# Optimization experiments

Hardware: AMD Instinct MI355X
Metric: run time of the kernel (lower is better)

The kernel has to match this reference:

```python
import jax, jax.numpy as jnp
import numpy as np

DIM = 2048
NUM_EXPERTS = 64
TOP_K = 2


def setup_inputs() -> dict:
    key = jax.random.key(0)
    kx, kw = jax.random.split(key)
    x = jax.random.normal(kx, (4, 8192, DIM), dtype=jnp.float32)
    # nn.Linear(dim, num_experts, bias=False) -> weight [num_experts, dim]
    W = jax.random.normal(kw, (NUM_EXPERTS, DIM), dtype=jnp.float32) * (1.0 / np.sqrt(DIM))
    return {"x": x, "W": W}


def reference(x, W):
    # gate scores: [B, S, E]
    gate_scores = jnp.einsum("bsd,ed->bse", x, W)
    # top-k over experts
    top_k_values, top_k_indices = jax.lax.top_k(gate_scores, TOP_K)
    top_k_weights = jax.nn.softmax(top_k_values, axis=-1)  # [B, S, K]
    # load-balancing aux loss
    expert_usage = jax.nn.softmax(gate_scores, axis=-1).mean(axis=(0, 1))  # [E]
    aux_loss = NUM_EXPERTS * jnp.sum(expert_usage ** 2)
    return (top_k_indices, top_k_weights, aux_loss)
```

## Files before the change

### kernel.cpp

```cpp
#include <hip/hip_runtime.h>

#define DIM   2048
#define NE    64
#define NTOK  32768
#define BM    64
#define NTHR  256
#define KW    (DIM/4)
#define BK    32
#define NKT   (KW/BK)
#define S     68

struct SmemGemm { float xs[4][BK*S]; float ws[4][BK*S]; };
struct SmemEpi  { float ps[4][BM*S]; float mx[BM]; float zinv[BM]; float us[4][NE]; };
union  Smem     { SmemGemm g; SmemEpi e; };

__global__ __launch_bounds__(NTHR, 2)
void router_main(const float* __restrict__ x, const float* __restrict__ W,
                 float* __restrict__ out_idx, float* __restrict__ out_w,
                 float* __restrict__ gusage)
{
    __shared__ Smem sm;
    const int tid  = threadIdx.x;
    const int w    = tid >> 6;
    const int ln   = tid & 63;
    const int tok0 = blockIdx.x * BM;
    const int a    = ln & 7;
    const int b    = ln >> 3;

    const float* xr = x + (size_t)(tok0 + ln) * DIM + w * KW;
    const float* wr = W + (size_t)ln * DIM + w * KW;

    float* xs = sm.g.xs[w];
    float* ws = sm.g.ws[w];

    float4 px[8], pw[8];
#pragma unroll
    for (int j = 0; j < 8; ++j) {
        px[j] = *(const float4*)(xr + 4*j);
        pw[j] = *(const float4*)(wr + 4*j);
    }

    float acc[8][8];
#pragma unroll
    for (int i = 0; i < 8; ++i)
#pragma unroll
        for (int jj = 0; jj < 8; ++jj) acc[i][jj] = 0.f;

    for (int kt = 0; kt < NKT; ++kt) {
#pragma unroll
        for (int j = 0; j < 8; ++j) {
            const int k = 4*j;
            xs[(k+0)*S + ln] = px[j].x;
            xs[(k+1)*S + ln] = px[j].y;
            xs[(k+2)*S + ln] = px[j].z;
            xs[(k+3)*S + ln] = px[j].w;
            ws[(k+0)*S + ln] = pw[j].x;
            ws[(k+1)*S + ln] = pw[j].y;
            ws[(k+2)*S + ln] = pw[j].z;
            ws[(k+3)*S + ln] = pw[j].w;
        }
        if (kt + 1 < NKT) {
            const int off = (kt + 1) * BK;
#pragma unroll
            for (int j = 0; j < 8; ++j) {
                px[j] = *(const float4*)(xr + off + 4*j);
                pw[j] = *(const float4*)(wr + off + 4*j);
            }
        }
#pragma unroll 4
        for (int dk = 0; dk < BK; ++dk) {
            const float4 a0 = *(const float4*)&xs[dk*S + 8*a];
            const float4 a1 = *(const float4*)&xs[dk*S + 8*a + 4];
            const float4 b0 = *(const float4*)&ws[dk*S + 8*b];
            const float4 b1 = *(const float4*)&ws[dk*S + 8*b + 4];
            const float av[8] = {a0.x,a0.y,a0.z,a0.w,a1.x,a1.y,a1.z,a1.w};
            const float bv[8] = {b0.x,b0.y,b0.z,b0.w,b1.x,b1.y,b1.z,b1.w};
#pragma unroll
            for (int i = 0; i < 8; ++i)
#pragma unroll
                for (int jj = 0; jj < 8; ++jj)
                    acc[i][jj] += av[i] * bv[jj];
        }
    }

    __syncthreads();
    {
        float* ps = sm.e.ps[w];
#pragma unroll
        for (int i = 0; i < 8; ++i) {
            *(float4*)&ps[(8*a+i)*S + 8*b    ] = make_float4(acc[i][0],acc[i][1],acc[i][2],acc[i][3]);
            *(float4*)&ps[(8*a+i)*S + 8*b + 4] = make_float4(acc[i][4],acc[i][5],acc[i][6],acc[i][7]);
        }
    }
    __syncthreads();
    {
        const int t = tid & 63;
        const int q = tid >> 6;
        float* p0 = sm.e.ps[0];
#pragma unroll
        for (int e0 = 0; e0 < 16; ++e0) {
            const int idx = t*S + (q*16 + e0);
            p0[idx] += sm.e.ps[1][idx] + sm.e.ps[2][idx] + sm.e.ps[3][idx];
        }
    }
    __syncthreads();

    const float* sc = sm.e.ps[0];
    if (tid < BM) {
        const int t = tid;
        float v1 = -3.4e38f, v2 = -3.4e38f;
        int   i1 = 0, i2 = 0;
        for (int e = 0; e < NE; ++e) {
            float s = sc[t*S + e];
            if (s > v1)      { v2 = v1; i2 = i1; v1 = s; i1 = e; }
            else if (s > v2) { v2 = s;  i2 = e; }
        }
        float z = 0.f;
        for (int e = 0; e < NE; ++e) z += __expf(sc[t*S + e] - v1);
        sm.e.mx[t]   = v1;
        sm.e.zinv[t] = 1.f / z;

        const int gt = tok0 + t;
        out_idx[gt*2 + 0] = (float)i1;
        out_idx[gt*2 + 1] = (float)i2;
        float e21 = __expf(v2 - v1);
        float w1  = 1.f / (1.f + e21);
        out_w[gt*2 + 0] = w1;
        out_w[gt*2 + 1] = e21 * w1;
    }
    __syncthreads();

    {
        const int e = tid & 63;
        const int c = tid >> 6;
        float u = 0.f;
        const int tbeg = c * 16;
        for (int t = tbeg; t < tbeg + 16; ++t)
            u += __expf(sc[t*S + e] - sm.e.mx[t]) * sm.e.zinv[t];
        sm.e.us[c][e] = u;
    }
    __syncthreads();
    if (tid < NE) {
        float u = sm.e.us[0][tid] + sm.e.us[1][tid] + sm.e.us[2][tid] + sm.e.us[3][tid];
        atomicAdd(&gusage[tid], u);
    }
}

__global__ void router_finalize(const float* __restrict__ gusage, float* __restrict__ out_aux)
{
    const int e = threadIdx.x;
    float u = gusage[e] * (1.0f / (float)NTOK);
    float s = u * u;
#pragma unroll
    for (int off = 32; off > 0; off >>= 1)
        s += __shfl_down(s, off, 64);
    if (e == 0) out_aux[0] = (float)NE * s;
}

extern "C" void kernel_launch(void* const* d_in, const int* in_sizes, int n_in,
                              void* d_out, int out_size, void* d_ws, size_t ws_size,
                              hipStream_t stream)
{
    const float* x = (const float*)d_in[0];
    const float* W = (const float*)d_in[1];
    float* out     = (float*)d_out;
    float* out_idx = out;
    float* out_w   = out + NTOK * 2;
    float* out_aux = out + NTOK * 4;
    float* gusage  = (float*)d_ws;

    hipMemsetAsync(d_ws, 0, NE * sizeof(float), stream);
    hipLaunchKernelGGL(router_main, dim3(NTOK / BM), dim3(NTHR), 0, stream,
                       x, W, out_idx, out_w, gusage);
    hipLaunchKernelGGL(router_finalize, dim3(1), dim3(NE), 0, stream, gusage, out_aux);
}
```

Baseline: 407.0 us.

## Use split-bf16 MFMA (bf16x3/6-term) for router GEMM instead of FP32 FMA

Replaces the scalar FP32 shared-memory GEMM with MFMA bf16 instructions. Both x and W are split into three bf16 parts (high, mid, low) and six cross products are accumulated, so results stay close to FP32 accuracy. W is pre-split once per call by a new kernel into workspace planes, while x is split on the fly in registers and loaded straight from global memory without shared-memory staging. This trades extra MFMA work, conversion ALU and an extra launch for matrix-core throughput, with a small risk to exact top-k tie ordering.

```diff
diff --git a/kernel.cpp b/kernel.cpp
--- a/kernel.cpp
+++ b/kernel.cpp
@@ -1,111 +1,169 @@
 #include <hip/hip_runtime.h>
 
-#define DIM   2048
-#define NE    64
-#define NTOK  32768
-#define BM    64
-#define NTHR  256
-#define KW    (DIM/4)
-#define BK    32
-#define NKT   (KW/BK)
-#define S     68
-
-struct SmemGemm { float xs[4][BK*S]; float ws[4][BK*S]; };
-struct SmemEpi  { float ps[4][BM*S]; float mx[BM]; float zinv[BM]; float us[4][NE]; };
-union  Smem     { SmemGemm g; SmemEpi e; };
+#define DIM    2048
+#define NE     64
+#define NTOK   32768
+#define BM     64
+#define NTHR   256
+#define KW     512
+#define NKC    16
+#define S      68
+#define WPLANE (NE*DIM)
+
+typedef __attribute__((ext_vector_type(8))) short short8;
+typedef __attribute__((ext_vector_type(4))) float f32x4;
+
+union U4S8 { uint4 u; short8 s; };
+
+__device__ __forceinline__ unsigned pack_hi16(unsigned e0, unsigned e1) {
+    return __builtin_amdgcn_perm(e1, e0, 0x07060302u);
+}
+
+__device__ __forceinline__ void split8(const float4& a, const float4& b,
+                                       short8& h, short8& m, short8& l) {
+    const float f[8] = {a.x, a.y, a.z, a.w, b.x, b.y, b.z, b.w};
+    unsigned hb[8], mb[8], lb[8];
+#pragma unroll
+    for (int j = 0; j < 8; ++j) {
+        const unsigned xb = __float_as_uint(f[j]);
+        const unsigned th = xb & 0xffff0000u;
+        const float    rh = f[j] - __uint_as_float(th);
+        const unsigned rb = __float_as_uint(rh);
+        const unsigned tm = rb & 0xffff0000u;
+        const float    rm = rh - __uint_as_float(tm);
+        hb[j] = th; mb[j] = tm; lb[j] = __float_as_uint(rm);
+    }
+    U4S8 H, M, L;
+    H.u = make_uint4(pack_hi16(hb[0],hb[1]), pack_hi16(hb[2],hb[3]),
+                     pack_hi16(hb[4],hb[5]), pack_hi16(hb[6],hb[7]));
+    M.u = make_uint4(pack_hi16(mb[0],mb[1]), pack_hi16(mb[2],mb[3]),
+                     pack_hi16(mb[4],mb[5]), pack_hi16(mb[6],mb[7]));
+    L.u = make_uint4(pack_hi16(lb[0],lb[1]), pack_hi16(lb[2],lb[3]),
+                     pack_hi16(lb[4],lb[5]), pack_hi16(lb[6],lb[7]));
+    h = H.s; m = M.s; l = L.s;
+}
+
+__global__ void router_wsplit(const float* __restrict__ W, unsigned short* __restrict__ W3)
+{
+    const int i = blockIdx.x * 256 + threadIdx.x;
+    const float f = W[i];
+    const unsigned xb = __float_as_uint(f);
+    const unsigned th = xb & 0xffff0000u;
+    const float    rh = f - __uint_as_float(th);
+    const unsigned rb = __float_as_uint(rh);
+    const unsigned tm = rb & 0xffff0000u;
+    const float    rm = rh - __uint_as_float(tm);
+    W3[i]            = (unsigned short)(th >> 16);
+    W3[WPLANE + i]   = (unsigned short)(tm >> 16);
+    W3[2*WPLANE + i] = (unsigned short)(__float_as_uint(rm) >> 16);
+}
+
+struct SmemEpi { float ps[4][BM * S]; float mx[BM]; float zinv[BM]; float us[4][NE]; };
+
+#define MFMA_GROUP(AF, BF)                                                       \
+    _Pragma("unroll") for (int nt = 0; nt < 4; ++nt)                             \
+    _Pragma("unroll") for (int mt = 0; mt < 4; ++mt)                             \
+        acc[mt][nt] = __builtin_amdgcn_mfma_f32_16x16x32_bf16(                   \
+            AF[mt], BF[nt].s, acc[mt][nt], 0, 0, 0);
 
 __global__ __launch_bounds__(NTHR, 2)
-void router_main(const float* __restrict__ x, const float* __restrict__ W,
+void router_main(const float* __restrict__ x, const unsigned short* __restrict__ W3,
                  float* __restrict__ out_idx, float* __restrict__ out_w,
                  float* __restrict__ gusage)
 {
-    __shared__ Smem sm;
+    __shared__ SmemEpi sm;
     const int tid  = threadIdx.x;
     const int w    = tid >> 6;
     const int ln   = tid & 63;
+    const int q    = ln >> 4;
+    const int c    = ln & 15;
     const int tok0 = blockIdx.x * BM;
-    const int a    = ln & 7;
-    const int b    = ln >> 3;
-
-    const float* xr = x + (size_t)(tok0 + ln) * DIM + w * KW;
-    const float* wr = W + (size_t)ln * DIM + w * KW;
-
-    float* xs = sm.g.xs[w];
-    float* ws = sm.g.ws[w];
-
-    float4 px[8], pw[8];
-#pragma unroll
-    for (int j = 0; j < 8; ++j) {
-        px[j] = *(const float4*)(xr + 4*j);
-        pw[j] = *(const float4*)(wr + 4*j);
-    }
-
-    float acc[8][8];
-#pragma unroll
-    for (int i = 0; i < 8; ++i)
-#pragma unroll
-        for (int jj = 0; jj < 8; ++jj) acc[i][jj] = 0.f;
-
-    for (int kt = 0; kt < NKT; ++kt) {
-#pragma unroll
-        for (int j = 0; j < 8; ++j) {
-            const int k = 4*j;
-            xs[(k+0)*S + ln] = px[j].x;
-            xs[(k+1)*S + ln] = px[j].y;
-            xs[(k+2)*S + ln] = px[j].z;
-            xs[(k+3)*S + ln] = px[j].w;
-            ws[(k+0)*S + ln] = pw[j].x;
-            ws[(k+1)*S + ln] = pw[j].y;
-            ws[(k+2)*S + ln] = pw[j].z;
-            ws[(k+3)*S + ln] = pw[j].w;
-        }
-        if (kt + 1 < NKT) {
-            const int off = (kt + 1) * BK;
-#pragma unroll
-            for (int j = 0; j < 8; ++j) {
-                px[j] = *(const float4*)(xr + off + 4*j);
-                pw[j] = *(const float4*)(wr + off + 4*j);
+    const int kbase = w * KW + q * 8;
+
+    const float* xr[4];
+#pragma unroll
+    for (int mt = 0; mt < 4; ++mt)
+        xr[mt] = x + (size_t)(tok0 + mt*16 + c) * DIM + kbase;
+    const unsigned short* wr[4];
+#pragma unroll
+    for (int nt = 0; nt < 4; ++nt)
+        wr[nt] = W3 + (size_t)(nt*16 + c) * DIM + kbase;
+
+    f32x4 acc[4][4];
+#pragma unroll
+    for (int mt = 0; mt < 4; ++mt)
+#pragma unroll
+        for (int nt = 0; nt < 4; ++nt)
+            acc[mt][nt] = (f32x4){0.f, 0.f, 0.f, 0.f};
+
+    float4 xf0[4], xf1[4];
+#pragma unroll
+    for (int mt = 0; mt < 4; ++mt) {
+        xf0[mt] = *(const float4*)(xr[mt]);
+        xf1[mt] = *(const float4*)(xr[mt] + 4);
+    }
+
+    for (int kc = 0; kc < NKC; ++kc) {
+        const int ko = kc * 32;
+        U4S8 bh[4];
+#pragma unroll
+        for (int nt = 0; nt < 4; ++nt) bh[nt].u = *(const uint4*)(wr[nt] + ko);
+
+        short8 ah[4], am[4], al[4];
+#pragma unroll
+        for (int mt = 0; mt < 4; ++mt) split8(xf0[mt], xf1[mt], ah[mt], am[mt], al[mt]);
+
+        if (kc + 1 < NKC) {
+#pragma unroll
+            for (int mt = 0; mt < 4; ++mt) {
+                xf0[mt] = *(const float4*)(xr[mt] + ko + 32);
+                xf1[mt] = *(const float4*)(xr[mt] + ko + 36);
             }
         }
-#pragma unroll 4
-        for (int dk = 0; dk < BK; ++dk) {
-            const float4 a0 = *(const float4*)&xs[dk*S + 8*a];
-            const float4 a1 = *(const float4*)&xs[dk*S + 8*a + 4];
-            const float4 b0 = *(const float4*)&ws[dk*S + 8*b];
-            const float4 b1 = *(const float4*)&ws[dk*S + 8*b + 4];
-            const float av[8] = {a0.x,a0.y,a0.z,a0.w,a1.x,a1.y,a1.z,a1.w};
-            const float bv[8] = {b0.x,b0.y,b0.z,b0.w,b1.x,b1.y,b1.z,b1.w};
-#pragma unroll
-            for (int i = 0; i < 8; ++i)
-#pragma unroll
-                for (int jj = 0; jj < 8; ++jj)
-                    acc[i][jj] += av[i] * bv[jj];
-        }
-    }
-
-    __syncthreads();
+
+        U4S8 bm[4];
+#pragma unroll
+        for (int nt = 0; nt < 4; ++nt) bm[nt].u = *(const uint4*)(wr[nt] + WPLANE + ko);
+
+        MFMA_GROUP(ah, bh)
+        MFMA_GROUP(am, bh)
+        MFMA_GROUP(al, bh)
+
+        U4S8 bl[4];
+#pragma unroll
+        for (int nt = 0; nt < 4; ++nt) bl[nt].u = *(const uint4*)(wr[nt] + 2*WPLANE + ko);
+
+        MFMA_GROUP(ah, bm)
+        MFMA_GROUP(am, bm)
+        MFMA_GROUP(ah, bl)
+    }
+
     {
-        float* ps = sm.e.ps[w];
-#pragma unroll
-        for (int i = 0; i < 8; ++i) {
-            *(float4*)&ps[(8*a+i)*S + 8*b    ] = make_float4(acc[i][0],acc[i][1],acc[i][2],acc[i][3]);
-            *(float4*)&ps[(8*a+i)*S + 8*b + 4] = make_float4(acc[i][4],acc[i][5],acc[i][6],acc[i][7]);
-        }
+        float* ps = sm.ps[w];
+#pragma unroll
+        for (int mt = 0; mt < 4; ++mt)
+#pragma unroll
+            for (int r = 0; r < 4; ++r) {
+                const int t = mt*16 + q*4 + r;
+#pragma unroll
+                for (int nt = 0; nt < 4; ++nt)
+                    ps[t*S + nt*16 + c] = acc[mt][nt][r];
+            }
     }
     __syncthreads();
     {
         const int t = tid & 63;
-        const int q = tid >> 6;
-        float* p0 = sm.e.ps[0];
+        const int qq = tid >> 6;
+        float* p0 = sm.ps[0];
 #pragma unroll
         for (int e0 = 0; e0 < 16; ++e0) {
-            const int idx = t*S + (q*16 + e0);
-            p0[idx] += sm.e.ps[1][idx] + sm.e.ps[2][idx] + sm.e.ps[3][idx];
+            const int idx = t*S + (qq*16 + e0);
+            p0[idx] += sm.ps[1][idx] + sm.ps[2][idx] + sm.ps[3][idx];
         }
     }
     __syncthreads();
 
-    const float* sc = sm.e.ps[0];
+    const float* sc = sm.ps[0];
     if (tid < BM) {
         const int t = tid;
         float v1 = -3.4e38f, v2 = -3.4e38f;
@@ -117,8 +175,8 @@
         }
         float z = 0.f;
         for (int e = 0; e < NE; ++e) z += __expf(sc[t*S + e] - v1);
-        sm.e.mx[t]   = v1;
-        sm.e.zinv[t] = 1.f / z;
+        sm.mx[t]   = v1;
+        sm.zinv[t] = 1.f / z;
 
         const int gt = tok0 + t;
         out_idx[gt*2 + 0] = (float)i1;
@@ -131,17 +189,17 @@
     __syncthreads();
 
     {
-        const int e = tid & 63;
-        const int c = tid >> 6;
+        const int e  = tid & 63;
+        const int cc = tid >> 6;
         float u = 0.f;
-        const int tbeg = c * 16;
+        const int tbeg = cc * 16;
         for (int t = tbeg; t < tbeg + 16; ++t)
-            u += __expf(sc[t*S + e] - sm.e.mx[t]) * sm.e.zinv[t];
-        sm.e.us[c][e] = u;
+            u += __expf(sc[t*S + e] - sm.mx[t]) * sm.zinv[t];
+        sm.us[cc][e] = u;
     }
     __syncthreads();
     if (tid < NE) {
-        float u = sm.e.us[0][tid] + sm.e.us[1][tid] + sm.e.us[2][tid] + sm.e.us[3][tid];
+        float u = sm.us[0][tid] + sm.us[1][tid] + sm.us[2][tid] + sm.us[3][tid];
         atomicAdd(&gusage[tid], u);
     }
 }
@@ -167,10 +225,13 @@
     float* out_idx = out;
     float* out_w   = out + NTOK * 2;
     float* out_aux = out + NTOK * 4;
-    float* gusage  = (float*)d_ws;
-
-    hipMemsetAsync(d_ws, 0, NE * sizeof(float), stream);
+
+    unsigned short* W3 = (unsigned short*)d_ws;
+    float* gusage = (float*)((char*)d_ws + 3 * WPLANE * sizeof(unsigned short));
+
+    hipMemsetAsync(gusage, 0, NE * sizeof(float), stream);
+    hipLaunchKernelGGL(router_wsplit, dim3(WPLANE / 256), dim3(256), 0, stream, W, W3);
     hipLaunchKernelGGL(router_main, dim3(NTOK / BM), dim3(NTHR), 0, stream,
-                       x, W, out_idx, out_w, gusage);
+                       x, W3, out_idx, out_w, gusage);
     hipLaunchKernelGGL(router_finalize, dim3(1), dim3(NE), 0, stream, gusage, out_aux);
 }
```

Measured after the change: 392.4 us. 1.04x faster.
